# Optimization experiments

Hardware: AMD Instinct MI355X
Metric: run time of the kernel (lower is better)

Reference implementation:

```python
import jax, jax.numpy as jnp
import numpy as np

B, T, D, H = 2, 2048, 768, 12
d = D // H
FRAG, K_SEL, G = 16, 6, 4
TOP_U, PROTO = 12, 32
ALPHA, GAMMA = 0.2, 0.2
W_MEAN, W_MAX, W_TOPK, W_STD = 1.0, 0.6, 0.4, 0.2
TOPK_FRAC = 0.2
TAU = 8.0
NEG = -1e9


def _norm(x, eps=1e-6):
    return x / jnp.maximum(jnp.linalg.norm(x, axis=-1, keepdims=True), eps)


def setup_inputs():
    key = jax.random.key(0)
    ks = jax.random.split(key, 5)
    s = 0.02
    return {
        'x': jax.random.normal(ks[0], (B, T, D), jnp.float32),
        'Wq': jax.random.normal(ks[1], (D, D), jnp.float32) * s,
        'bq': jnp.zeros((D,), jnp.float32),
        'Wk': jax.random.normal(ks[2], (D, D), jnp.float32) * s,
        'bk': jnp.zeros((D,), jnp.float32),
        'Wv': jax.random.normal(ks[3], (D, D), jnp.float32) * s,
        'bv': jnp.zeros((D,), jnp.float32),
        'Wo': jax.random.normal(ks[4], (D, D), jnp.float32) * s,
        'bo': jnp.zeros((D,), jnp.float32),
    }


def _forward(x, Wq, bq, Wk, bk, Wv, bv, Wo, bo):
    scaling = d ** -0.5

    def shape(t):  # [B,T,D] -> [B*H,T,d]  (BartAttention._shape layout: (b,h))
        return t.reshape(B, T, H, d).transpose(0, 2, 1, 3).reshape(B * H, T, d)

    q = shape((x @ Wq.T + bq) * scaling)
    k = shape(x @ Wk.T + bk)
    v = shape(x @ Wv.T + bv)

    # ---- windowed local candidate indices (build_indices_encoder) ----
    half = FRAG // 2
    t_ar = jnp.arange(T)
    starts = jnp.clip(t_ar - half, 0, T - FRAG)
    idx = starts[:, None] + jnp.arange(FRAG)[None, :]            # [T,F]
    prior = jnp.exp(-jnp.abs(idx - t_ar[:, None]).astype(jnp.float32) / TAU)

    keys_win = k[:, idx]                                          # [BH,T,F,d]
    scores_win = jnp.einsum('btd,btfd->btf', q, keys_win)
    blended = scores_win + ALPHA * prior[None]

    # ---- greedy diversity-penalized top-k (WindowSelector.select_greedy) ----
    kvn = _norm(keys_win)
    f_ar = jnp.arange(FRAG)
    tmp = blended
    sels = []
    for r in range(K_SEL):
        j = jnp.argmax(tmp, -1)                                   # [BH,T]
        sels.append(j)
        if r < K_SEL - 1:
            sel_vec = jnp.take_along_axis(kvn, j[:, :, None, None], axis=2)[:, :, 0]
            cos = jnp.maximum(jnp.sum(kvn * sel_vec[:, :, None, :], -1), 0.0)
            tmp = tmp - GAMMA * cos
        tmp = jnp.where(f_ar[None, None, :] == j[..., None], NEG, tmp)
    sel_local = jnp.stack(sels, -1)                               # [BH,T,k]
    sel_abs = jnp.take_along_axis(
        jnp.broadcast_to(idx[None], (B * H, T, FRAG)), sel_local, axis=-1)

    # ---- per-head global tokens (GlobalChooser.choose_packed) ----
    # faithful to torch: key_states.view(H, bsz, Tk, d).mean(dim=1)
    Kmean = k.reshape(H, B, T, d).mean(1)
    Kbar = _norm(Kmean)
    q_summary = _norm(q.reshape(H, B, T, d).mean(1))
    idxp = jnp.round(jnp.linspace(0.0, T - 1, PROTO)).astype(jnp.int32)
    Qp = q_summary[:, idxp]                                       # [H,P,d]
    S = jax.nn.relu(jnp.einsum('hkd,hpd->hkp', Kbar, Qp))         # [H,T,P]
    kq = max(1, int(round(PROTO * TOPK_FRAC)))
    u = (W_MEAN * S.mean(-1) + W_MAX * S.max(-1)
         + W_TOPK * jax.lax.top_k(S, kq)[0].mean(-1)
         + W_STD * jnp.std(S, axis=-1, ddof=1))
    U = min(TOP_U, T)
    u_vals, top_idx = jax.lax.top_k(u, U)                         # [H,U]
    S_sub = jnp.take_along_axis(S, top_idx[:, :, None], axis=1)   # [H,U,P]
    hr = jnp.arange(H)
    m = jnp.zeros((H, PROTO), S.dtype)
    blocked = jnp.zeros((H, U), bool)
    chosen = []
    for r in range(G):  # greedy facility-location
        gains = jnp.maximum(S_sub - m[:, None, :], 0.0).sum(-1)
        gains = jnp.where(blocked, NEG, gains)
        j = jnp.argmax(gains, 1)
        chosen.append(j)
        blocked = blocked.at[hr, j].set(True)
        m = jnp.maximum(m, S_sub[hr, j])
    chosen_abs = jnp.take_along_axis(top_idx, jnp.stack(chosen, 1), axis=1)  # [H,G]

    # ---- sparse attention over local + global candidates ----
    glob = jnp.broadcast_to(chosen_abs[None], (B, H, G)).reshape(B * H, G)
    cand = jnp.concatenate(
        [sel_abs, jnp.broadcast_to(glob[:, None, :], (B * H, T, G))], -1)  # [BH,T,k+g]
    Ksel = jax.vmap(lambda kk, ii: kk[ii])(k, cand)               # [BH,T,k+g,d]
    Vsel = jax.vmap(lambda vv, ii: vv[ii])(v, cand)
    attn = jax.nn.softmax(jnp.einsum('btd,btcd->btc', q, Ksel), axis=-1)
    out = jnp.einsum('btc,btcd->btd', attn, Vsel)
    out = out.reshape(B, H, T, d).transpose(0, 2, 1, 3).reshape(B, T, D)
    return out @ Wo.T + bo


def reference(x, Wq, bq, Wk, bk, Wv, bv, Wo, bo):
    return _forward(x, Wq, bq, Wk, bk, Wv, bv, Wo, bo)
```

## Files before the change

kernel.cpp:

```cpp
#include <hip/hip_runtime.h>
#include <math.h>

#define TSEQ 2048
#define DM   768
#define NH   12
#define HD   64
#define NBH  24
#define WN   589824

typedef __attribute__((ext_vector_type(8))) short short8;
typedef __attribute__((ext_vector_type(8))) _Float16 half8;
typedef __attribute__((ext_vector_type(4))) float f32x4;

#define MFMA_BF16(a, b, c) __builtin_amdgcn_mfma_f32_16x16x32_bf16(a, b, c, 0, 0, 0)
#define MFMA_F16(a, b, c)  __builtin_amdgcn_mfma_f32_16x16x32_f16(a, b, c, 0, 0, 0)

__constant__ int c_idxp[32] = {0,66,132,198,264,330,396,462,528,594,660,726,
  792,858,924,990,1057,1123,1189,1255,1321,1387,1453,1519,1585,1651,1717,1783,
  1849,1915,1981,2047};

template <int CTRL>
__device__ __forceinline__ float dppf(float x) {
  return __int_as_float(__builtin_amdgcn_mov_dpp(__float_as_int(x), CTRL, 0xF, 0xF, true));
}
template <int CTRL>
__device__ __forceinline__ int dppi(int x) {
  return __builtin_amdgcn_mov_dpp(x, CTRL, 0xF, 0xF, true);
}
__device__ __forceinline__ float wsum(float v) {
  v += dppf<0x121>(v);
  v += dppf<0x122>(v);
  v += dppf<0x124>(v);
  v += dppf<0x128>(v);
  v += __shfl_xor(v, 16, 64);
  v += __shfl_xor(v, 32, 64);
  return v;
}
__device__ __forceinline__ float wmaxr(float v) {
  v = fmaxf(v, dppf<0x121>(v));
  v = fmaxf(v, dppf<0x122>(v));
  v = fmaxf(v, dppf<0x124>(v));
  v = fmaxf(v, dppf<0x128>(v));
  v = fmaxf(v, __shfl_xor(v, 16, 64));
  v = fmaxf(v, __shfl_xor(v, 32, 64));
  return v;
}

__device__ __forceinline__ ushort bf16rne(float x) {
  unsigned u = __float_as_uint(x);
  return (ushort)((u + 0x7fffu + ((u >> 16) & 1u)) >> 16);
}

__device__ __forceinline__ void split16(const float4& v0, const float4& v1,
                                        ushort* ph, ushort* pl) {
  float xs[8] = {v0.x, v0.y, v0.z, v0.w, v1.x, v1.y, v1.z, v1.w};
  half8 h, l;
#pragma unroll
  for (int j = 0; j < 8; ++j) {
    _Float16 hb = (_Float16)xs[j];
    h[j] = hb;
    float d = xs[j] - (float)hb;
    l[j] = (_Float16)d;
  }
  *(half8*)ph = h;
  *(half8*)pl = l;
}

__device__ __forceinline__ int lds_idx(int row, int chunk ) {
  int line = row >> 1;
  int c8 = ((row & 1) << 2) | chunk;
  return line * 64 + ((c8 ^ (line & 7)) << 3);
}

__global__ __launch_bounds__(256) void convert_kernel(
    const float* __restrict__ x,
    const float* __restrict__ W0, const float* __restrict__ W1,
    const float* __restrict__ W2, const float* __restrict__ W3,
    ushort* __restrict__ Xh, ushort* __restrict__ Xl,
    ushort* __restrict__ wsp) {
  int z = blockIdx.y;
  size_t base = (size_t)(blockIdx.x * 256 + threadIdx.x) * 8;
  if (z == 0) {
    float4 v0 = *(const float4*)(x + base);
    float4 v1 = *(const float4*)(x + base + 4);
    split16(v0, v1, Xh + base, Xl + base);
  } else {
    if (base >= WN) return;
    int mi = z - 1;
    const float* s = (mi == 0) ? W0 : (mi == 1) ? W1 : (mi == 2) ? W2 : W3;
    ushort* h = wsp + (size_t)mi * 2 * WN;
    float4 v0 = *(const float4*)(s + base);
    float4 v1 = *(const float4*)(s + base + 4);
    split16(v0, v1, h + base, h + WN + base);
  }
}

template <int MODE, int NPROD>
__device__ __forceinline__ void gemm_mfma_body(
    const ushort* __restrict__ Agh, const ushort* __restrict__ Agl,
    const ushort* __restrict__ Bgh, const ushort* __restrict__ Bgl,
    const float* __restrict__ bias, float* __restrict__ dst, float scale,
    int mblk, int nblk, ushort* lds) {
  const int tid = threadIdx.x;
  const int lane = tid & 63;
  const int w = tid >> 6;
  const int wr = w >> 1, wc = w & 1;
  const int lrow = lane & 15, kq = lane >> 4;
  constexpr int ABUF = 4096;
  constexpr int BBUF = 2048;
  ushort* Ahs = lds;
  ushort* Als = Ahs + ABUF;
  ushort* Bhs = lds + 2 * ABUF;
  ushort* Bls = Bhs + BBUF;

  const int arow = tid >> 2;
  const int achk = tid & 3;
  const int aoff0 = lds_idx(arow, achk);
  const int aoff1 = lds_idx(arow + 64, achk);
  const int boff = lds_idx(arow, achk);

  const size_t a0 = (size_t)(mblk + arow) * DM + achk * 8;
  const size_t a1 = (size_t)(mblk + 64 + arow) * DM + achk * 8;
  const size_t b0 = (size_t)(nblk + arow) * DM + achk * 8;

  f32x4 acc[4][2];
#pragma unroll
  for (int i = 0; i < 4; ++i)
#pragma unroll
    for (int j = 0; j < 2; ++j) {
      f32x4 z = {0.f, 0.f, 0.f, 0.f};
      acc[i][j] = z;
    }

  short8 pah0 = *(const short8*)(Agh + a0), pah1 = *(const short8*)(Agh + a1);
  short8 pal0 = *(const short8*)(Agl + a0), pal1 = *(const short8*)(Agl + a1);
  short8 pbh = *(const short8*)(Bgh + b0);
  short8 pbl = *(const short8*)(Bgl + b0);

  for (int k0 = 0; k0 < DM; k0 += 32) {
    __syncthreads();
    *(short8*)&Ahs[aoff0] = pah0; *(short8*)&Ahs[aoff1] = pah1;
    *(short8*)&Als[aoff0] = pal0; *(short8*)&Als[aoff1] = pal1;
    *(short8*)&Bhs[boff] = pbh;
    *(short8*)&Bls[boff] = pbl;
    __syncthreads();
    if (k0 + 32 < DM) {
      pah0 = *(const short8*)(Agh + a0 + k0 + 32);
      pah1 = *(const short8*)(Agh + a1 + k0 + 32);
      pal0 = *(const short8*)(Agl + a0 + k0 + 32);
      pal1 = *(const short8*)(Agl + a1 + k0 + 32);
      pbh = *(const short8*)(Bgh + b0 + k0 + 32);
      pbl = *(const short8*)(Bgl + b0 + k0 + 32);
    }
    half8 afh[4], afl[4];
#pragma unroll
    for (int fi = 0; fi < 4; ++fi) {
      int o = lds_idx(wr * 64 + fi * 16 + lrow, kq);
      afh[fi] = *(const half8*)&Ahs[o];
      afl[fi] = *(const half8*)&Als[o];
    }
#pragma unroll
    for (int fj = 0; fj < 2; ++fj) {
      int o = lds_idx(wc * 32 + fj * 16 + lrow, kq);
      half8 bfh = *(const half8*)&Bhs[o];
      half8 bfl = *(const half8*)&Bls[o];
#pragma unroll
      for (int fi = 0; fi < 4; ++fi) {
        acc[fi][fj] = MFMA_F16(afh[fi], bfh, acc[fi][fj]);
        acc[fi][fj] = MFMA_F16(afl[fi], bfh, acc[fi][fj]);
        acc[fi][fj] = MFMA_F16(afh[fi], bfl, acc[fi][fj]);
        if (NPROD == 4) {
          acc[fi][fj] = MFMA_F16(afl[fi], bfl, acc[fi][fj]);
        }
      }
    }
  }

#pragma unroll
  for (int fj = 0; fj < 2; ++fj) {
    int col = nblk + wc * 32 + fj * 16 + lrow;
    float bv = bias[col];
#pragma unroll
    for (int fi = 0; fi < 4; ++fi) {
#pragma unroll
      for (int reg = 0; reg < 4; ++reg) {
        int row = mblk + wr * 64 + fi * 16 + kq * 4 + reg;
        float o = (acc[fi][fj][reg] + bv) * scale;
        if (MODE == 0) {
          dst[(size_t)row * DM + col] = o;
        } else {
          int b_ = row >> 11, t = row & (TSEQ - 1);
          int h = col >> 6, dd = col & 63;
          dst[(((size_t)(b_ * NH + h)) * TSEQ + t) * HD + dd] = o;
        }
      }
    }
  }
}

__global__ __launch_bounds__(256) void qkv_kernel(
    const ushort* __restrict__ Xh, const ushort* __restrict__ Xl,
    const ushort* __restrict__ wsp,
    const float* __restrict__ bq, float* __restrict__ qd,
    const float* __restrict__ bk, float* __restrict__ kd,
    const float* __restrict__ bv, float* __restrict__ vd) {
  __shared__ ushort lds[2 * 4096 + 2 * 2048];
  int lid = blockIdx.x + 12 * blockIdx.y + 384 * blockIdx.z;
  int swz = (lid & 7) * 144 + (lid >> 3);
  int z = swz / 384;
  int rem = swz - z * 384;
  int wy = rem / 12, wx = rem - wy * 12;
  const ushort* Bb = wsp + (size_t)z * 2 * WN;
  if (z == 2) {
    gemm_mfma_body<1, 3>(Xh, Xl, Bb, Bb + WN,
                         bv, vd, 1.0f, wy * 128, wx * 64, lds);
  } else {
    gemm_mfma_body<1, 4>(Xh, Xl, Bb, Bb + WN,
                         z ? bk : bq, z ? kd : qd, z ? 1.0f : 0.125f,
                         wy * 128, wx * 64, lds);
  }
}

__global__ __launch_bounds__(256) void oproj_kernel(
    const ushort* __restrict__ Ph, const ushort* __restrict__ Pl,
    const ushort* __restrict__ wsp,
    const float* __restrict__ bias, float* __restrict__ dst) {
  __shared__ ushort lds[2 * 4096 + 2 * 2048];
  int lid = blockIdx.x + 12 * blockIdx.y;
  int swz = (lid & 7) * 48 + (lid >> 3);
  int wy = swz / 12, wx = swz - wy * 12;
  const ushort* Bb = wsp + (size_t)3 * 2 * WN;
  gemm_mfma_body<0, 3>(Ph, Pl, Bb, Bb + WN,
                       bias, dst, 1.0f, wy * 128, wx * 64, lds);
}

__global__ __launch_bounds__(256) void window_kernel(
    const float* __restrict__ q, const float* __restrict__ k,
    int* __restrict__ sel) {
  int wid = blockIdx.x * 4 + (threadIdx.x >> 6);
  int lane = threadIdx.x & 63;
  int f = lane & 15, kq = lane >> 4;
  int bh = wid >> 11, t = wid & (TSEQ - 1);
  int start = t - 8;
  if (start < 0) start = 0;
  if (start > TSEQ - 16) start = TSEQ - 16;

  const float* kp = k + ((size_t)bh * TSEQ + start + f) * HD + kq * 8;
  const float* qp = q + ((size_t)bh * TSEQ + t) * HD + kq * 8;
  float kv[16], qv[16];
  *(float4*)&kv[0]  = *(const float4*)(kp + 0);
  *(float4*)&kv[4]  = *(const float4*)(kp + 4);
  *(float4*)&kv[8]  = *(const float4*)(kp + 32);
  *(float4*)&kv[12] = *(const float4*)(kp + 36);
  *(float4*)&qv[0]  = *(const float4*)(qp + 0);
  *(float4*)&qv[4]  = *(const float4*)(qp + 4);
  *(float4*)&qv[8]  = *(const float4*)(qp + 32);
  *(float4*)&qv[12] = *(const float4*)(qp + 36);

  float sp = 0.f, np = 0.f;
#pragma unroll
  for (int i = 0; i < 16; ++i) { sp = fmaf(qv[i], kv[i], sp); np = fmaf(kv[i], kv[i], np); }
  sp += __shfl_xor(sp, 16, 64); sp += __shfl_xor(sp, 32, 64);
  np += __shfl_xor(np, 16, 64); np += __shfl_xor(np, 32, 64);
  float nrm = fmaxf(sqrtf(np), 1e-6f);
  float kn[16];
#pragma unroll
  for (int i = 0; i < 16; ++i) kn[i] = kv[i] / nrm;

  short8 h0, m0, l0, h1, m1, l1;
#pragma unroll
  for (int j = 0; j < 8; ++j) {
    float x = kn[j];
    ushort hb = bf16rne(x); h0[j] = (short)hb;
    float d = x - __uint_as_float((unsigned)hb << 16);
    ushort mb = bf16rne(d); m0[j] = (short)mb;
    l0[j] = (short)bf16rne(d - __uint_as_float((unsigned)mb << 16));
    x = kn[8 + j];
    hb = bf16rne(x); h1[j] = (short)hb;
    d = x - __uint_as_float((unsigned)hb << 16);
    mb = bf16rne(d); m1[j] = (short)mb;
    l1[j] = (short)bf16rne(d - __uint_as_float((unsigned)mb << 16));
  }
  f32x4 g = {0.f, 0.f, 0.f, 0.f};
  g = MFMA_BF16(h0, h0, g); g = MFMA_BF16(h1, h1, g);
  g = MFMA_BF16(m0, h0, g); g = MFMA_BF16(m1, h1, g);
  g = MFMA_BF16(h0, m0, g); g = MFMA_BF16(h1, m1, g);
  g = MFMA_BF16(m0, m0, g); g = MFMA_BF16(m1, m1, g);
  g = MFMA_BF16(l0, h0, g); g = MFMA_BF16(l1, h1, g);
  g = MFMA_BF16(h0, l0, g); g = MFMA_BF16(h1, l1, g);

  int dist = start + f - t; if (dist < 0) dist = -dist;
  float tmp = sp + 0.2f * expf(-(float)dist * 0.125f);

  int* selp = sel + ((size_t)bh * TSEQ + t) * 6;
#pragma unroll
  for (int r = 0; r < 6; ++r) {
    float best = tmp; int bj = f;
    {
      float ov = dppf<0x121>(best); int oi = dppi<0x121>(bj);
      if (ov > best || (ov == best && oi < bj)) { best = ov; bj = oi; }
      ov = dppf<0x122>(best); oi = dppi<0x122>(bj);
      if (ov > best || (ov == best && oi < bj)) { best = ov; bj = oi; }
      ov = dppf<0x124>(best); oi = dppi<0x124>(bj);
      if (ov > best || (ov == best && oi < bj)) { best = ov; bj = oi; }
      ov = dppf<0x128>(best); oi = dppi<0x128>(bj);
      if (ov > best || (ov == best && oi < bj)) { best = ov; bj = oi; }
    }
    if (lane == 0) selp[r] = start + bj;
    if (r < 5) {
      float s01 = (bj & 1) ? g[1] : g[0];
      float s23 = (bj & 1) ? g[3] : g[2];
      float gsel = (bj & 2) ? s23 : s01;
      float grow = __shfl(gsel, ((bj >> 2) << 4) | f, 64);
      tmp -= 0.2f * fmaxf(grow, 0.f);
    }
    if (f == bj) tmp = -1e9f;
  }
}

__global__ __launch_bounds__(256) void qp_kernel(const float* __restrict__ q,
                                                 float* __restrict__ Qp) {
  int wid = blockIdx.x * 4 + (threadIdx.x >> 6);
  int lane = threadIdx.x & 63;
  int a = wid >> 5, p = wid & 31;
  int t = c_idxp[p];
  float v = 0.5f * (q[((size_t)(2 * a) * TSEQ + t) * HD + lane] +
                    q[((size_t)(2 * a + 1) * TSEQ + t) * HD + lane]);
  float n2 = wsum(v * v);
  float nrm = fmaxf(sqrtf(n2), 1e-6f);
  Qp[((size_t)a * 32 + p) * HD + lane] = v / nrm;
}

__global__ __launch_bounds__(256) void proto_score_kernel(
    const float* __restrict__ k, const float* __restrict__ Qp,
    float* __restrict__ S, float* __restrict__ u) {
  int a = blockIdx.y;
  __shared__ float Qs[2048];
  for (int i = threadIdx.x; i < 2048; i += 256) Qs[i] = Qp[(size_t)a * 2048 + i];
  __syncthreads();
  int w = threadIdx.x >> 6, lane = threadIdx.x & 63;
  int t = blockIdx.x * 4 + w;
  float km = 0.5f * (k[((size_t)(2 * a) * TSEQ + t) * HD + lane] +
                     k[((size_t)(2 * a + 1) * TSEQ + t) * HD + lane]);
  float n2 = wsum(km * km);
  float nrm = fmaxf(sqrtf(n2), 1e-6f);
  float kb = km / nrm;
  float sval = 0.f;
#pragma unroll
  for (int p = 0; p < 32; ++p) {
    float dg = wsum(kb * Qs[p * 64 + lane]);
    dg = fmaxf(dg, 0.f);
    sval = (lane == p) ? dg : sval;
  }
  if (lane < 32) S[((size_t)a * TSEQ + t) * 32 + lane] = sval;
  float x = (lane < 32) ? sval : 0.f;
  float mean = wsum(x) / 32.0f;
  float mx = wmaxr((lane < 32) ? sval : -1e30f);
  float cur = (lane < 32) ? sval : -1e30f;
  float topsum = 0.f;
#pragma unroll
  for (int r = 0; r < 6; ++r) {
    float m = wmaxr(cur);
    topsum += m;
    unsigned long long ball = __ballot(cur == m);
    int first = __ffsll(ball) - 1;
    if (lane == first) cur = -1e30f;
  }
  float dev = (lane < 32) ? (sval - mean) : 0.f;
  float sd = sqrtf(wsum(dev * dev) / 31.0f);
  float uval = ((1.0f * mean + 0.6f * mx) + 0.4f * (topsum / 6.0f)) + 0.2f * sd;
  if (lane == 0) u[(size_t)a * TSEQ + t] = uval;
}

__global__ void head_select_kernel(const float* __restrict__ u,
                                   const float* __restrict__ S,
                                   int* __restrict__ glob) {
  int a = blockIdx.x;
  int lane = threadIdx.x;
  float uv[32];
#pragma unroll
  for (int c = 0; c < 32; ++c) uv[c] = u[(size_t)a * TSEQ + c * 64 + lane];
  unsigned removed = 0;
  int tidx = 0;
#pragma unroll
  for (int r = 0; r < 12; ++r) {
    float best = -1e30f; int bidx = 1 << 30;
#pragma unroll
    for (int c = 0; c < 32; ++c) {
      if (!((removed >> c) & 1u)) {
        float vv = uv[c]; int gi = c * 64 + lane;
        if (vv > best || (vv == best && gi < bidx)) { best = vv; bidx = gi; }
      }
    }
#pragma unroll
    for (int mS = 1; mS < 64; mS <<= 1) {
      float ov = __shfl_xor(best, mS, 64);
      int oi = __shfl_xor(bidx, mS, 64);
      if (ov > best || (ov == best && oi < bidx)) { best = ov; bidx = oi; }
    }
    if (lane == (bidx & 63)) removed |= 1u << (bidx >> 6);
    if (lane == r) tidx = bidx;
  }
  float srow[12];
#pragma unroll
  for (int r = 0; r < 12; ++r) {
    int tr = __shfl(tidx, r, 64);
    srow[r] = (lane < 32) ? S[((size_t)a * TSEQ + tr) * 32 + lane] : 0.f;
  }
  float m = 0.f;
  unsigned blocked = 0;
#pragma unroll
  for (int g = 0; g < 4; ++g) {
    float gains[12];
#pragma unroll
    for (int r = 0; r < 12; ++r) {
      float gr = (lane < 32) ? fmaxf(srow[r] - m, 0.f) : 0.f;
      gains[r] = wsum(gr);
    }
    float best = -1e30f; int bj = 0;
#pragma unroll
    for (int r = 0; r < 12; ++r) {
      float vv = ((blocked >> r) & 1u) ? -1e9f : gains[r];
      if (vv > best) { best = vv; bj = r; }
    }
    blocked |= 1u << bj;
#pragma unroll
    for (int r = 0; r < 12; ++r) m = (r == bj) ? fmaxf(m, srow[r]) : m;
    int gidx = __shfl(tidx, bj, 64);
    if (lane == 0) glob[a * 4 + g] = gidx;
  }
}

__global__ __launch_bounds__(256) void attend_kernel(
    const float* __restrict__ q, const float* __restrict__ k,
    const float* __restrict__ v, const int* __restrict__ sel,
    const int* __restrict__ glob, ushort* __restrict__ Ph,
    ushort* __restrict__ Pl) {
  int wid = blockIdx.x * 4 + (threadIdx.x >> 6);
  int lane = threadIdx.x & 63;
  int bh = wid >> 11, t = wid & (TSEQ - 1);
  int h = bh % NH, b = bh / NH;
  float qv = q[((size_t)bh * TSEQ + t) * HD + lane];
  int cand[10];
  const int* selp = sel + ((size_t)bh * TSEQ + t) * 6;
#pragma unroll
  for (int c = 0; c < 6; ++c) cand[c] = selp[c];
#pragma unroll
  for (int c = 0; c < 4; ++c) cand[6 + c] = glob[h * 4 + c];
  float sc[10];
#pragma unroll
  for (int c = 0; c < 10; ++c) {
    float kv = k[((size_t)bh * TSEQ + cand[c]) * HD + lane];
    sc[c] = wsum(qv * kv);
  }
  float mx = sc[0];
#pragma unroll
  for (int c = 1; c < 10; ++c) mx = fmaxf(mx, sc[c]);
  float e[10], den = 0.f;
#pragma unroll
  for (int c = 0; c < 10; ++c) { e[c] = expf(sc[c] - mx); den += e[c]; }
  float o = 0.f;
#pragma unroll
  for (int c = 0; c < 10; ++c) {
    float w = e[c] / den;
    o += w * v[((size_t)bh * TSEQ + cand[c]) * HD + lane];
  }
  size_t idx = ((size_t)b * TSEQ + t) * DM + h * HD + lane;
  _Float16 hb = (_Float16)o;
  float d = o - (float)hb;
  Ph[idx] = __builtin_bit_cast(ushort, hb);
  _Float16 lb = (_Float16)d;
  Pl[idx] = __builtin_bit_cast(ushort, lb);
}

extern "C" void kernel_launch(void* const* d_in, const int* in_sizes, int n_in,
                              void* d_out, int out_size, void* d_ws, size_t ws_size,
                              hipStream_t stream) {
  const float* x  = (const float*)d_in[0];
  const float* Wq = (const float*)d_in[1];
  const float* bq = (const float*)d_in[2];
  const float* Wk = (const float*)d_in[3];
  const float* bk = (const float*)d_in[4];
  const float* Wv = (const float*)d_in[5];
  const float* bv = (const float*)d_in[6];
  const float* Wo = (const float*)d_in[7];
  const float* bo = (const float*)d_in[8];
  float* out = (float*)d_out;

  float* ws = (float*)d_ws;
  const size_t QKV = (size_t)NBH * TSEQ * HD;
  float* qb = ws;
  float* kb = qb + QKV;
  float* vb = kb + QKV;
  float* slotA = vb + QKV;
  float* Qp = slotA + QKV;
  float* S  = Qp + (size_t)NH * 32 * HD;
  float* u  = S + (size_t)NH * TSEQ * 32;
  int* sel  = (int*)(u + (size_t)NH * TSEQ);
  int* glob = sel + (size_t)NBH * TSEQ * 6;
  ushort* wsp = (ushort*)(glob + 64);

  ushort* Xh = (ushort*)slotA;
  ushort* Xl = Xh + QKV;
  ushort* Ph = Xh;
  ushort* Pl = Xl;

  convert_kernel<<<dim3(1536, 5), 256, 0, stream>>>(
      x, Wq, Wk, Wv, Wo, Xh, Xl, wsp);
  qkv_kernel<<<dim3(12, 32, 3), 256, 0, stream>>>(
      Xh, Xl, wsp, bq, qb, bk, kb, bv, vb);
  window_kernel<<<12288, 256, 0, stream>>>(qb, kb, sel);
  qp_kernel<<<96, 256, 0, stream>>>(qb, Qp);
  proto_score_kernel<<<dim3(512, NH), 256, 0, stream>>>(kb, Qp, S, u);
  head_select_kernel<<<NH, 64, 0, stream>>>(u, S, glob);
  attend_kernel<<<12288, 256, 0, stream>>>(qb, kb, vb, sel, glob, Ph, Pl);
  oproj_kernel<<<dim3(12, 32), 256, 0, stream>>>(Ph, Pl, wsp, bo, out);
}
```

Before: 243.6 us.

## Use split-fp16 MFMA for prototype scores and window Gram matrix

The prototype-scoring kernel switches from per-wavefront scalar dot products with 32 cross-lane reductions per token to split-fp16 (hi/lo) MFMA tiles. Each wave now scores 16 tokens against 32 prototypes, so the grid shrinks from 512 to 32 blocks per head. The per-token statistics (mean, max, top-6, std) are rebuilt with 16-lane DPP row reductions. The window kernel's Gram matrix moves from a three-term bf16 split with 12 MFMAs to a two-term fp16 split with 8 MFMAs, which cuts instruction count but may change precision and greedy tie-breaking.

```diff
diff --git a/kernel.cpp b/kernel.cpp
--- a/kernel.cpp
+++ b/kernel.cpp
@@ -12,7 +12,6 @@
 typedef __attribute__((ext_vector_type(8))) _Float16 half8;
 typedef __attribute__((ext_vector_type(4))) float f32x4;
 
-#define MFMA_BF16(a, b, c) __builtin_amdgcn_mfma_f32_16x16x32_bf16(a, b, c, 0, 0, 0)
 #define MFMA_F16(a, b, c)  __builtin_amdgcn_mfma_f32_16x16x32_f16(a, b, c, 0, 0, 0)
 
 __constant__ int c_idxp[32] = {0,66,132,198,264,330,396,462,528,594,660,726,
@@ -45,10 +44,20 @@
   v = fmaxf(v, __shfl_xor(v, 32, 64));
   return v;
 }
-
-__device__ __forceinline__ ushort bf16rne(float x) {
-  unsigned u = __float_as_uint(x);
-  return (ushort)((u + 0x7fffu + ((u >> 16) & 1u)) >> 16);
+__device__ __forceinline__ float rowsum16(float v) {
+  v += dppf<0x121>(v); v += dppf<0x122>(v);
+  v += dppf<0x124>(v); v += dppf<0x128>(v);
+  return v;
+}
+__device__ __forceinline__ float rowmax16(float v) {
+  v = fmaxf(v, dppf<0x121>(v)); v = fmaxf(v, dppf<0x122>(v));
+  v = fmaxf(v, dppf<0x124>(v)); v = fmaxf(v, dppf<0x128>(v));
+  return v;
+}
+__device__ __forceinline__ int rowmin16i(int v) {
+  v = min(v, dppi<0x121>(v)); v = min(v, dppi<0x122>(v));
+  v = min(v, dppi<0x124>(v)); v = min(v, dppi<0x128>(v));
+  return v;
 }
 
 __device__ __forceinline__ void split16(const float4& v0, const float4& v1,
@@ -70,6 +79,9 @@
   int line = row >> 1;
   int c8 = ((row & 1) << 2) | chunk;
   return line * 64 + ((c8 ^ (line & 7)) << 3);
+}
+__device__ __forceinline__ int qoff(int p, int c8) {
+  return p * 64 + (((c8 ^ (p & 7)) & 7) << 3);
 }
 
 __global__ __launch_bounds__(256) void convert_kernel(
@@ -267,27 +279,21 @@
 #pragma unroll
   for (int i = 0; i < 16; ++i) kn[i] = kv[i] / nrm;
 
-  short8 h0, m0, l0, h1, m1, l1;
+  half8 h0, l0, h1, l1;
 #pragma unroll
   for (int j = 0; j < 8; ++j) {
-    float x = kn[j];
-    ushort hb = bf16rne(x); h0[j] = (short)hb;
-    float d = x - __uint_as_float((unsigned)hb << 16);
-    ushort mb = bf16rne(d); m0[j] = (short)mb;
-    l0[j] = (short)bf16rne(d - __uint_as_float((unsigned)mb << 16));
-    x = kn[8 + j];
-    hb = bf16rne(x); h1[j] = (short)hb;
-    d = x - __uint_as_float((unsigned)hb << 16);
-    mb = bf16rne(d); m1[j] = (short)mb;
-    l1[j] = (short)bf16rne(d - __uint_as_float((unsigned)mb << 16));
+    _Float16 hb = (_Float16)kn[j];
+    h0[j] = hb;
+    l0[j] = (_Float16)(kn[j] - (float)hb);
+    _Float16 hb1 = (_Float16)kn[8 + j];
+    h1[j] = hb1;
+    l1[j] = (_Float16)(kn[8 + j] - (float)hb1);
   }
   f32x4 g = {0.f, 0.f, 0.f, 0.f};
-  g = MFMA_BF16(h0, h0, g); g = MFMA_BF16(h1, h1, g);
-  g = MFMA_BF16(m0, h0, g); g = MFMA_BF16(m1, h1, g);
-  g = MFMA_BF16(h0, m0, g); g = MFMA_BF16(h1, m1, g);
-  g = MFMA_BF16(m0, m0, g); g = MFMA_BF16(m1, m1, g);
-  g = MFMA_BF16(l0, h0, g); g = MFMA_BF16(l1, h1, g);
-  g = MFMA_BF16(h0, l0, g); g = MFMA_BF16(h1, l1, g);
+  g = MFMA_F16(h0, h0, g); g = MFMA_F16(h1, h1, g);
+  g = MFMA_F16(l0, h0, g); g = MFMA_F16(l1, h1, g);
+  g = MFMA_F16(h0, l0, g); g = MFMA_F16(h1, l1, g);
+  g = MFMA_F16(l0, l0, g); g = MFMA_F16(l1, l1, g);
 
   int dist = start + f - t; if (dist < 0) dist = -dist;
   float tmp = sp + 0.2f * expf(-(float)dist * 0.125f);
@@ -319,7 +325,8 @@
 }
 
 __global__ __launch_bounds__(256) void qp_kernel(const float* __restrict__ q,
-                                                 float* __restrict__ Qp) {
+                                                 ushort* __restrict__ Qph,
+                                                 ushort* __restrict__ Qpl) {
   int wid = blockIdx.x * 4 + (threadIdx.x >> 6);
   int lane = threadIdx.x & 63;
   int a = wid >> 5, p = wid & 31;
@@ -328,48 +335,112 @@
                     q[((size_t)(2 * a + 1) * TSEQ + t) * HD + lane]);
   float n2 = wsum(v * v);
   float nrm = fmaxf(sqrtf(n2), 1e-6f);
-  Qp[((size_t)a * 32 + p) * HD + lane] = v / nrm;
+  float qn = v / nrm;
+  _Float16 hb = (_Float16)qn;
+  float d = qn - (float)hb;
+  size_t idx = ((size_t)a * 32 + p) * HD + lane;
+  Qph[idx] = __builtin_bit_cast(ushort, hb);
+  _Float16 lb = (_Float16)d;
+  Qpl[idx] = __builtin_bit_cast(ushort, lb);
 }
 
 __global__ __launch_bounds__(256) void proto_score_kernel(
-    const float* __restrict__ k, const float* __restrict__ Qp,
+    const float* __restrict__ k,
+    const ushort* __restrict__ Qph, const ushort* __restrict__ Qpl,
     float* __restrict__ S, float* __restrict__ u) {
   int a = blockIdx.y;
-  __shared__ float Qs[2048];
-  for (int i = threadIdx.x; i < 2048; i += 256) Qs[i] = Qp[(size_t)a * 2048 + i];
+  __shared__ ushort Qh[2048], Ql[2048];
+  {
+    int p = threadIdx.x >> 3, c8 = threadIdx.x & 7;
+    size_t src = (size_t)a * 2048 + p * 64 + c8 * 8;
+    *(short8*)&Qh[qoff(p, c8)] = *(const short8*)(Qph + src);
+    *(short8*)&Ql[qoff(p, c8)] = *(const short8*)(Qpl + src);
+  }
   __syncthreads();
-  int w = threadIdx.x >> 6, lane = threadIdx.x & 63;
-  int t = blockIdx.x * 4 + w;
-  float km = 0.5f * (k[((size_t)(2 * a) * TSEQ + t) * HD + lane] +
-                     k[((size_t)(2 * a + 1) * TSEQ + t) * HD + lane]);
-  float n2 = wsum(km * km);
-  float nrm = fmaxf(sqrtf(n2), 1e-6f);
-  float kb = km / nrm;
-  float sval = 0.f;
-#pragma unroll
-  for (int p = 0; p < 32; ++p) {
-    float dg = wsum(kb * Qs[p * 64 + lane]);
-    dg = fmaxf(dg, 0.f);
-    sval = (lane == p) ? dg : sval;
-  }
-  if (lane < 32) S[((size_t)a * TSEQ + t) * 32 + lane] = sval;
-  float x = (lane < 32) ? sval : 0.f;
-  float mean = wsum(x) / 32.0f;
-  float mx = wmaxr((lane < 32) ? sval : -1e30f);
-  float cur = (lane < 32) ? sval : -1e30f;
-  float topsum = 0.f;
-#pragma unroll
-  for (int r = 0; r < 6; ++r) {
-    float m = wmaxr(cur);
-    topsum += m;
-    unsigned long long ball = __ballot(cur == m);
-    int first = __ffsll(ball) - 1;
-    if (lane == first) cur = -1e30f;
-  }
-  float dev = (lane < 32) ? (sval - mean) : 0.f;
-  float sd = sqrtf(wsum(dev * dev) / 31.0f);
-  float uval = ((1.0f * mean + 0.6f * mx) + 0.4f * (topsum / 6.0f)) + 0.2f * sd;
-  if (lane == 0) u[(size_t)a * TSEQ + t] = uval;
+
+  int wv = threadIdx.x >> 6, lane = threadIdx.x & 63;
+  int f = lane & 15, kq = lane >> 4;
+  int tbase = blockIdx.x * 64 + wv * 16;
+  int tl = tbase + f;
+
+  const float* k0p = k + ((size_t)(2 * a) * TSEQ + tl) * HD + kq * 8;
+  const float* k1p = k + ((size_t)(2 * a + 1) * TSEQ + tl) * HD + kq * 8;
+  float km[16];
+  {
+    float4 x0 = *(const float4*)(k0p + 0),  y0 = *(const float4*)(k1p + 0);
+    float4 x1 = *(const float4*)(k0p + 4),  y1 = *(const float4*)(k1p + 4);
+    float4 x2 = *(const float4*)(k0p + 32), y2 = *(const float4*)(k1p + 32);
+    float4 x3 = *(const float4*)(k0p + 36), y3 = *(const float4*)(k1p + 36);
+    km[0] = 0.5f*(x0.x+y0.x); km[1] = 0.5f*(x0.y+y0.y);
+    km[2] = 0.5f*(x0.z+y0.z); km[3] = 0.5f*(x0.w+y0.w);
+    km[4] = 0.5f*(x1.x+y1.x); km[5] = 0.5f*(x1.y+y1.y);
+    km[6] = 0.5f*(x1.z+y1.z); km[7] = 0.5f*(x1.w+y1.w);
+    km[8] = 0.5f*(x2.x+y2.x); km[9] = 0.5f*(x2.y+y2.y);
+    km[10] = 0.5f*(x2.z+y2.z); km[11] = 0.5f*(x2.w+y2.w);
+    km[12] = 0.5f*(x3.x+y3.x); km[13] = 0.5f*(x3.y+y3.y);
+    km[14] = 0.5f*(x3.z+y3.z); km[15] = 0.5f*(x3.w+y3.w);
+  }
+  float np = 0.f;
+#pragma unroll
+  for (int i = 0; i < 16; ++i) np = fmaf(km[i], km[i], np);
+  np += __shfl_xor(np, 16, 64); np += __shfl_xor(np, 32, 64);
+  float nrm = fmaxf(sqrtf(np), 1e-6f);
+
+  half8 ah[2], al[2];
+#pragma unroll
+  for (int s = 0; s < 2; ++s)
+#pragma unroll
+    for (int j = 0; j < 8; ++j) {
+      float x = km[s * 8 + j] / nrm;
+      _Float16 hb = (_Float16)x;
+      ah[s][j] = hb;
+      al[s][j] = (_Float16)(x - (float)hb);
+    }
+
+  f32x4 acc0 = {0.f, 0.f, 0.f, 0.f}, acc1 = {0.f, 0.f, 0.f, 0.f};
+#pragma unroll
+  for (int s = 0; s < 2; ++s) {
+    half8 b0h = *(const half8*)&Qh[qoff(f, s * 4 + kq)];
+    half8 b0l = *(const half8*)&Ql[qoff(f, s * 4 + kq)];
+    half8 b1h = *(const half8*)&Qh[qoff(16 + f, s * 4 + kq)];
+    half8 b1l = *(const half8*)&Ql[qoff(16 + f, s * 4 + kq)];
+    acc0 = MFMA_F16(ah[s], b0h, acc0);
+    acc0 = MFMA_F16(al[s], b0h, acc0);
+    acc0 = MFMA_F16(ah[s], b0l, acc0);
+    acc0 = MFMA_F16(al[s], b0l, acc0);
+    acc1 = MFMA_F16(ah[s], b1h, acc1);
+    acc1 = MFMA_F16(al[s], b1h, acc1);
+    acc1 = MFMA_F16(ah[s], b1l, acc1);
+    acc1 = MFMA_F16(al[s], b1l, acc1);
+  }
+
+#pragma unroll
+  for (int reg = 0; reg < 4; ++reg) {
+    float s0 = fmaxf(acc0[reg], 0.f);
+    float s1 = fmaxf(acc1[reg], 0.f);
+    int t = tbase + kq * 4 + reg;
+    size_t srow = ((size_t)a * TSEQ + t) * 32;
+    S[srow + f] = s0;
+    S[srow + 16 + f] = s1;
+    float mean = rowsum16(s0 + s1) / 32.0f;
+    float mx = rowmax16(fmaxf(s0, s1));
+    float cur0 = s0, cur1 = s1;
+    float topsum = 0.f;
+#pragma unroll
+    for (int r = 0; r < 6; ++r) {
+      float mm = rowmax16(fmaxf(cur0, cur1));
+      topsum += mm;
+      int i0 = rowmin16i((cur0 == mm) ? f : 999);
+      int i1 = rowmin16i((cur1 == mm) ? f : 999);
+      bool take0 = (i0 < 999);
+      if (take0 && f == i0) cur0 = -1e30f;
+      if (!take0 && f == i1) cur1 = -1e30f;
+    }
+    float d0 = s0 - mean, d1 = s1 - mean;
+    float sd = sqrtf(rowsum16(d0 * d0 + d1 * d1) / 31.0f);
+    float uval = ((1.0f * mean + 0.6f * mx) + 0.4f * (topsum / 6.0f)) + 0.2f * sd;
+    if (f == 0) u[(size_t)a * TSEQ + t] = uval;
+  }
 }
 
 __global__ void head_select_kernel(const float* __restrict__ u,
@@ -493,8 +564,8 @@
   float* kb = qb + QKV;
   float* vb = kb + QKV;
   float* slotA = vb + QKV;
-  float* Qp = slotA + QKV;
-  float* S  = Qp + (size_t)NH * 32 * HD;
+  float* QpSlot = slotA + QKV;
+  float* S  = QpSlot + (size_t)NH * 32 * HD;
   float* u  = S + (size_t)NH * TSEQ * 32;
   int* sel  = (int*)(u + (size_t)NH * TSEQ);
   int* glob = sel + (size_t)NBH * TSEQ * 6;
@@ -504,14 +575,16 @@
   ushort* Xl = Xh + QKV;
   ushort* Ph = Xh;
   ushort* Pl = Xl;
+  ushort* Qph = (ushort*)QpSlot;
+  ushort* Qpl = Qph + (size_t)NH * 32 * HD;
 
   convert_kernel<<<dim3(1536, 5), 256, 0, stream>>>(
       x, Wq, Wk, Wv, Wo, Xh, Xl, wsp);
   qkv_kernel<<<dim3(12, 32, 3), 256, 0, stream>>>(
       Xh, Xl, wsp, bq, qb, bk, kb, bv, vb);
   window_kernel<<<12288, 256, 0, stream>>>(qb, kb, sel);
-  qp_kernel<<<96, 256, 0, stream>>>(qb, Qp);
-  proto_score_kernel<<<dim3(512, NH), 256, 0, stream>>>(kb, Qp, S, u);
+  qp_kernel<<<96, 256, 0, stream>>>(qb, Qph, Qpl);
+  proto_score_kernel<<<dim3(32, NH), 256, 0, stream>>>(kb, Qph, Qpl, S, u);
   head_select_kernel<<<NH, 64, 0, stream>>>(u, S, glob);
   attend_kernel<<<12288, 256, 0, stream>>>(qb, kb, vb, sel, glob, Ph, Pl);
   oproj_kernel<<<dim3(12, 32), 256, 0, stream>>>(Ph, Pl, wsp, bo, out);
```

Result: faster. 217.1 us (-10.9%).
